# Performance work log

Measured on AMD Instinct MI355X. Metric: run time of the kernel, lower is better.

Reference implementation:

```python
import jax, jax.numpy as jnp
import numpy as np

B, Z, K, T = 4, 64, 400, 48000
CIN, COUT, KS, DIL = 128, 128, 3, 1
H = 32


def setup_inputs() -> dict:
    key = jax.random.key(0)
    ks = jax.random.split(key, 10)
    s = lambda n: 1.0 / np.sqrt(n)
    return {
        "x": jax.random.normal(ks[0], (B, CIN, T), jnp.float32),
        "z": jax.random.normal(ks[1], (B, Z, K), jnp.float32),
        # weight_model: Conv1d(Z->H, k=1), ReLU, Conv1d(H -> CIN*COUT*KS, k=1)
        "w1": jax.random.normal(ks[2], (H, Z), jnp.float32) * s(Z),
        "b1": jax.random.normal(ks[3], (H,), jnp.float32) * 0.01,
        "w2": jax.random.normal(ks[4], (CIN * COUT * KS, H), jnp.float32) * s(H),
        "b2": jax.random.normal(ks[5], (CIN * COUT * KS,), jnp.float32) * s(CIN * KS),
        # bias_model: Conv1d(Z->H, k=1), ReLU, Conv1d(H -> COUT, k=1)
        "bw1": jax.random.normal(ks[6], (H, Z), jnp.float32) * s(Z),
        "bb1": jax.random.normal(ks[7], (H,), jnp.float32) * 0.01,
        "bw2": jax.random.normal(ks[8], (COUT, H), jnp.float32) * s(H),
        "bb2": jax.random.normal(ks[9], (COUT,), jnp.float32) * 0.01,
    }


def _mlp1x1(z, wa, ba, wb, bb):
    # two pointwise Conv1d layers with ReLU in between; z: [B, Z, K]
    h = jax.nn.relu(jnp.einsum('hz,bzk->bhk', wa, z) + ba[None, :, None])
    return jnp.einsum('oh,bhk->bok', wb, h) + bb[None, :, None]


def _unfold_causal(x, ksize, dil):
    # causal im2col: tap i is x delayed by i*dil samples (left-padded with zeros)
    pad = dil * (ksize - 1)
    xp = jnp.pad(x, ((0, 0), (0, 0), (pad, 0)))
    taps = [xp[:, :, pad - i * dil: pad - i * dil + x.shape[-1]] for i in range(ksize)]
    return jnp.concatenate(taps, axis=1)  # [B, CIN*KS, T]


def reference(x, z, w1, b1, w2, b2, bw1, bb1, bw2, bb2):
    Tk = T // K  # samples per weight chunk
    xu = _unfold_causal(x, KS, DIL)                       # [B, CIN*KS, T]
    xr = xu.transpose(0, 2, 1).reshape(B * K, Tk, CIN * KS)
    w = _mlp1x1(z, w1, b1, w2, b2)                        # [B, CIN*COUT*KS, K]
    w = w.reshape(B, CIN * KS, COUT, K).transpose(0, 3, 1, 2).reshape(B * K, CIN * KS, COUT)
    bias = _mlp1x1(z, bw1, bb1, bw2, bb2)                 # [B, COUT, K]
    bias = bias.transpose(0, 2, 1).reshape(B * K, COUT)
    y = jnp.einsum('btc,bco->bto', xr, w) + bias[:, None, :]
    return y.reshape(B, T, COUT).transpose(0, 2, 1)       # [B, COUT, T]
```

## Files before the change

kernel.cpp:

```cpp
#include <hip/hip_runtime.h>
#include <stdint.h>

#define TT     48000
#define TK     120
#define NC     128
#define NA     384
#define NZ     64
#define NH     32
#define NK     400
#define NCHUNK 1600
#define MW     49152
#define XROWS  48002

typedef float f32x4 __attribute__((ext_vector_type(4)));
typedef __bf16 bf16x8 __attribute__((ext_vector_type(8)));

static __device__ __forceinline__ uint16_t f2bf(float f) {
    uint32_t x; __builtin_memcpy(&x, &f, 4);
    return (uint16_t)((x + 0x7fffu + ((x >> 16) & 1u)) >> 16);
}
static __device__ __forceinline__ uint32_t pk2(uint16_t lo, uint16_t hi) {
    return (uint32_t)lo | ((uint32_t)hi << 16);
}

__global__ __launch_bounds__(256) void k0w(
    const float* __restrict__ w2, const float* __restrict__ b2,
    uint16_t* __restrict__ w2p, float* __restrict__ b2p) {
    int m = blockIdx.x * 256 + threadIdx.x;
    int a = m >> 7, c = m & 127;
    int mp = c * NA + a;
    const float* src = w2 + (size_t)m * NH;
    uint16_t* dst = w2p + (size_t)mp * NH;
#pragma unroll
    for (int i = 0; i < NH; i += 8) {
        float4 v0 = *(const float4*)(src + i);
        float4 v1 = *(const float4*)(src + i + 4);
        uint4 o;
        o.x = pk2(f2bf(v0.x), f2bf(v0.y));
        o.y = pk2(f2bf(v0.z), f2bf(v0.w));
        o.z = pk2(f2bf(v1.x), f2bf(v1.y));
        o.w = pk2(f2bf(v1.z), f2bf(v1.w));
        *(uint4*)(dst + i) = o;
    }
    b2p[mp] = b2[m];
}

__global__ __launch_bounds__(256) void k0x(
    const float* __restrict__ x, uint16_t* __restrict__ Xt) {
    int t0 = blockIdx.x * 128, cin0 = blockIdx.y * 64, b = blockIdx.z;
    int tid = threadIdx.x;
    __shared__ __align__(16) uint16_t Lt[128][72];
    const float* xb = x + ((size_t)b * NC + cin0) * TT + t0;
    int cg = (tid & 7) * 8;
    int tq = (tid >> 3) * 4;
    uint16_t vb[4][8];
#pragma unroll
    for (int i = 0; i < 8; ++i) {
        float4 v = *(const float4*)(xb + (size_t)(cg + i) * TT + tq);
        vb[0][i] = f2bf(v.x); vb[1][i] = f2bf(v.y);
        vb[2][i] = f2bf(v.z); vb[3][i] = f2bf(v.w);
    }
#pragma unroll
    for (int j = 0; j < 4; ++j) {
        uint4 o; __builtin_memcpy(&o, vb[j], 16);
        *(uint4*)&Lt[tq + j][cg] = o;
    }
    __syncthreads();
    uint16_t* XtB = Xt + (size_t)b * XROWS * NC;
#pragma unroll
    for (int r = 0; r < 4; ++r) {
        int s = r * 256 + tid;
        int t = s >> 3, cc = s & 7;
        uint4 o = *(uint4*)&Lt[t][cc * 8];
        *(uint4*)(XtB + (size_t)(t0 + t + 2) * NC + cin0 + cc * 8) = o;
    }
    if (blockIdx.x == 0 && blockIdx.y == 0 && tid < 32)
        *(uint4*)(XtB + tid * 8) = make_uint4(0, 0, 0, 0);
}

__global__ __launch_bounds__(256) void k1_hidden(
    const float* __restrict__ z,
    const float* __restrict__ w1, const float* __restrict__ b1,
    const float* __restrict__ bw1, const float* __restrict__ bb1,
    const float* __restrict__ bw2, const float* __restrict__ bb2,
    uint16_t* __restrict__ Hb, float* __restrict__ biasws) {
    int tid = threadIdx.x, lane = tid & 63, w = tid >> 6;
    int chunk0 = blockIdx.x * 4;
    int b = chunk0 / NK;
    int k0 = chunk0 - b * NK;

    __shared__ float w1sT[64][33];
    __shared__ float bw1sT[64][33];
    __shared__ float bw2s[128][33];
    __shared__ float zs[64][4];
    __shared__ float hbs[4][33];
    __shared__ float b1s[32], bb1s[32], bb2s[128];

    {
        int row = tid >> 3, c0 = (tid & 7) * 8;
        float4 a0 = *(const float4*)(w1 + row * NZ + c0);
        float4 a1 = *(const float4*)(w1 + row * NZ + c0 + 4);
        float4 c0v = *(const float4*)(bw1 + row * NZ + c0);
        float4 c1v = *(const float4*)(bw1 + row * NZ + c0 + 4);
        const float av[8] = {a0.x,a0.y,a0.z,a0.w,a1.x,a1.y,a1.z,a1.w};
        const float cv[8] = {c0v.x,c0v.y,c0v.z,c0v.w,c1v.x,c1v.y,c1v.z,c1v.w};
#pragma unroll
        for (int j = 0; j < 8; ++j) {
            w1sT[c0 + j][row]  = av[j];
            bw1sT[c0 + j][row] = cv[j];
        }
    }
    {
        int r = tid >> 1, cb = (tid & 1) * 16;
        float4 v0 = *(const float4*)(bw2 + r * NH + cb);
        float4 v1 = *(const float4*)(bw2 + r * NH + cb + 4);
        float4 v2 = *(const float4*)(bw2 + r * NH + cb + 8);
        float4 v3 = *(const float4*)(bw2 + r * NH + cb + 12);
        const float vv[16] = {v0.x,v0.y,v0.z,v0.w,v1.x,v1.y,v1.z,v1.w,
                              v2.x,v2.y,v2.z,v2.w,v3.x,v3.y,v3.z,v3.w};
#pragma unroll
        for (int j = 0; j < 16; ++j) bw2s[r][cb + j] = vv[j];
    }
    if (tid < 64) {
        float4 zv = *(const float4*)(z + ((size_t)b * NZ + tid) * NK + k0);
        zs[tid][0] = zv.x; zs[tid][1] = zv.y; zs[tid][2] = zv.z; zs[tid][3] = zv.w;
    }
    if (tid < 32) { b1s[tid] = b1[tid]; bb1s[tid] = bb1[tid]; }
    if (tid >= 128 && tid < 256) bb2s[tid - 128] = bb2[tid - 128];
    __syncthreads();

    int chunk = chunk0 + w;
    if (lane < NH) {
        float s = b1s[lane];
#pragma unroll
        for (int i = 0; i < NZ; ++i) s = fmaf(w1sT[i][lane], zs[i][w], s);
        Hb[(size_t)chunk * NH + lane] = f2bf(fmaxf(s, 0.f));
    } else {
        int j = lane - NH;
        float s = bb1s[j];
#pragma unroll
        for (int i = 0; i < NZ; ++i) s = fmaf(bw1sT[i][j], zs[i][w], s);
        hbs[w][j] = fmaxf(s, 0.f);
    }

#pragma unroll
    for (int r = 0; r < 2; ++r) {
        int c = r * 64 + lane;
        float s = bb2s[c];
#pragma unroll
        for (int j = 0; j < NH; ++j) s = fmaf(bw2s[c][j], hbs[w][j], s);
        biasws[(size_t)chunk * NC + c] = s;
    }
}

__global__ __launch_bounds__(256) void k2_wgen(
    const uint16_t* __restrict__ w2p, const float* __restrict__ b2p,
    const uint16_t* __restrict__ Hb, uint16_t* __restrict__ Wt,
    int chunk0, int nchunk) {
    int tid = threadIdx.x, lane = tid & 63, w = tid >> 6;
    int quad = lane >> 4, li = lane & 15;
    __shared__ __align__(16) uint16_t St[4][16][68];
    int mb = blockIdx.x * 256 + w * 64;

    bf16x8 afrag[4];
    float4 bias[4];
#pragma unroll
    for (int t = 0; t < 4; ++t) {
        afrag[t] = *(const bf16x8*)(w2p + (size_t)(mb + t * 16 + li) * NH + quad * 8);
        bias[t]  = *(const float4*)(b2p + mb + t * 16 + quad * 4);
    }

    for (int g = 0; g < 10; ++g) {
        int cl0 = blockIdx.y * 160 + g * 16;
        if (cl0 >= nchunk) break;
        int cl = cl0 + li;
        if (cl >= nchunk) cl = nchunk - 1;
        bf16x8 hfrag = *(const bf16x8*)(Hb + (size_t)(chunk0 + cl) * NH + quad * 8);
#pragma unroll
        for (int t = 0; t < 4; ++t) {
            f32x4 acc = {0.f, 0.f, 0.f, 0.f};
            acc = __builtin_amdgcn_mfma_f32_16x16x32_bf16(afrag[t], hfrag, acc, 0, 0, 0);
            uint16_t p[4] = { f2bf(acc[0] + bias[t].x), f2bf(acc[1] + bias[t].y),
                              f2bf(acc[2] + bias[t].z), f2bf(acc[3] + bias[t].w) };
            uint64_t pv; __builtin_memcpy(&pv, p, 8);
            *(uint64_t*)&St[w][li][t * 16 + quad * 4] = pv;
        }
#pragma unroll
        for (int p = 0; p < 2; ++p) {
            int ch = (lane >> 3) + p * 8, part = lane & 7;
            uint4 v = *(const uint4*)&St[w][ch][part * 8];
            int cg = cl0 + ch;
            if (cg < nchunk)
                *(uint4*)(Wt + (size_t)cg * MW + mb + part * 8) = v;
        }
    }
}

__global__ __launch_bounds__(256) void k3_conv(
    const uint16_t* __restrict__ Xt, const uint16_t* __restrict__ Wt,
    const float* __restrict__ biasws, float* __restrict__ out, int chunk0) {
    int cl = blockIdx.x, chunk = chunk0 + cl;
    int b = chunk / NK, k = chunk - b * NK;
    int kbase = k * TK;
    int tid = threadIdx.x, lane = tid & 63, w = tid >> 6;
    int quad = lane >> 4, li = lane & 15;
    int tblk = (w & 1) * 64, cblk = (w >> 1) * 64;

    __shared__ __align__(16) char smem[65536];
    char* Xa  = smem;
    char* Db0 = smem + 32768;
    char* Db1 = smem + 49152;
    const uint16_t* XtB = Xt + (size_t)b * XROWS * NC;
    const uint16_t* WtC = Wt + (size_t)cl * MW;

    f32x4 acc[4][4];
#pragma unroll
    for (int i = 0; i < 4; ++i)
#pragma unroll
        for (int j = 0; j < 4; ++j) acc[i][j] = (f32x4){0.f, 0.f, 0.f, 0.f};

    auto stageD = [&](char* dst, int dks) {
#pragma unroll
        for (int j = 0; j < 4; ++j) {
            int g = (w * 4 + j) * 64 + lane;
            int c = g >> 3, sd = g & 7;
            int o = sd ^ (c & 7);
            const uint16_t* gsrc = WtC + (size_t)c * NA + dks * 64 + o * 8;
            __builtin_amdgcn_global_load_lds(
                (__attribute__((address_space(1))) void*)gsrc,
                (__attribute__((address_space(3))) void*)(dst + (w * 4 + j) * 1024),
                16, 0, 0);
        }
    };

#pragma unroll
    for (int i = 0; i < 8; ++i) {
        int brow = w * 32 + i * 4 + quad;
        const uint16_t* g = XtB + (size_t)(kbase + brow) * NC
                          + ((li ^ (brow & 15)) * 8);
        __builtin_amdgcn_global_load_lds(
            (__attribute__((address_space(1))) void*)g,
            (__attribute__((address_space(3))) void*)(Xa + (w * 32 + i * 4) * 256),
            16, 0, 0);
    }
    stageD(Db0, 0);

#pragma unroll
    for (int dk = 0; dk < 6; ++dk) {
        __syncthreads();
        if (dk < 5) stageD((dk & 1) ? Db0 : Db1, dk + 1);
        char* cur = (dk & 1) ? Db1 : Db0;
        int tap = dk >> 1;

        bf16x8 bfr[2][4];
#pragma unroll
        for (int s = 0; s < 2; ++s)
#pragma unroll
            for (int ct = 0; ct < 4; ++ct) {
                int c = cblk + ct * 16 + li;
                bfr[s][ct] = *(const bf16x8*)(cur + c * 128
                             + (((s * 4 + quad) ^ (c & 7)) << 4));
            }
#pragma unroll
        for (int s = 0; s < 2; ++s) {
            bf16x8 af[4];
#pragma unroll
            for (int tt = 0; tt < 4; ++tt) {
                int r = tblk + tt * 16 + li + 2 - tap;
                r = r > 127 ? 127 : r;
                int q = (dk & 1) * 8 + s * 4 + quad;
                af[tt] = *(const bf16x8*)(Xa + r * 256 + ((q ^ (r & 15)) << 4));
            }
#pragma unroll
            for (int tt = 0; tt < 4; ++tt)
#pragma unroll
                for (int ct = 0; ct < 4; ++ct)
                    acc[tt][ct] = __builtin_amdgcn_mfma_f32_16x16x32_bf16(
                        af[tt], bfr[s][ct], acc[tt][ct], 0, 0, 0);
        }
    }

#pragma unroll
    for (int ct = 0; ct < 4; ++ct) {
        int c = cblk + ct * 16 + li;
        float bias = biasws[(size_t)chunk * NC + c];
        float* ob = out + ((size_t)b * NC + c) * TT + kbase;
#pragma unroll
        for (int tt = 0; tt < 4; ++tt) {
            int t0v = tblk + tt * 16 + quad * 4;
            if (t0v < TK) {
                f32x4 v = acc[tt][ct];
                *(float4*)(ob + t0v) = make_float4(v[0] + bias, v[1] + bias,
                                                   v[2] + bias, v[3] + bias);
            }
        }
    }
}

extern "C" void kernel_launch(void* const* d_in, const int* in_sizes, int n_in,
                              void* d_out, int out_size, void* d_ws, size_t ws_size,
                              hipStream_t stream) {
    const float* x   = (const float*)d_in[0];
    const float* z   = (const float*)d_in[1];
    const float* w1  = (const float*)d_in[2];
    const float* b1  = (const float*)d_in[3];
    const float* w2  = (const float*)d_in[4];
    const float* b2  = (const float*)d_in[5];
    const float* bw1 = (const float*)d_in[6];
    const float* bb1 = (const float*)d_in[7];
    const float* bw2 = (const float*)d_in[8];
    const float* bb2 = (const float*)d_in[9];
    float* out = (float*)d_out;

    char* ws = (char*)d_ws;
    uint16_t* Hb     = (uint16_t*)(ws);
    float*    biasws = (float*)(ws + 102400);
    uint16_t* w2p    = (uint16_t*)(ws + 921600);
    float*    b2p    = (float*)(ws + 4067328);
    uint16_t* Xt     = (uint16_t*)(ws + 4263936);
    const size_t wt_off = 53422080;
    uint16_t* Wt     = (uint16_t*)(ws + wt_off);

    size_t avail = (ws_size > wt_off) ? (ws_size - wt_off) : 0;
    int batch = (int)(avail / ((size_t)MW * 2));
    if (batch > 800) batch = 800;
    if (batch < 1) batch = 1;

    k0w<<<MW / 256, 256, 0, stream>>>(w2, b2, w2p, b2p);
    k0x<<<dim3(TT / 128, 2, 4), 256, 0, stream>>>(x, Xt);
    k1_hidden<<<NCHUNK / 4, 256, 0, stream>>>(z, w1, b1, bw1, bb1, bw2, bb2, Hb, biasws);

    for (int c0 = 0; c0 < NCHUNK; c0 += batch) {
        int nc = NCHUNK - c0;
        if (nc > batch) nc = batch;
        dim3 g2(MW / 256, (nc + 159) / 160, 1);
        k2_wgen<<<g2, 256, 0, stream>>>(w2p, b2p, Hb, Wt, c0, nc);
        k3_conv<<<nc, 256, 0, stream>>>(Xt, Wt, biasws, out, c0);
    }
}
```

Baseline: 292.3 us.

## Fuse weight repack into wgen, triple-buffer conv weight staging, raise batch cap

Removes the separate k0w repack kernel; k2_wgen now reads fp32 w2/b2 directly with a permuted index and converts to bf16 in registers. k3_conv moves from double to triple buffering of weight tiles, using explicit vmcnt waits plus raw s_barrier so each load is issued two steps ahead. The chunk batch cap rises to the full chunk count, which can cut the number of kernel launch pairs but makes the Wt buffer larger. The extra LDS (80KB) may reduce occupancy, and the strided fp32 reads in wgen may be less efficient.

```diff
diff --git a/kernel.cpp b/kernel.cpp
--- a/kernel.cpp
+++ b/kernel.cpp
@@ -19,31 +19,6 @@
     uint32_t x; __builtin_memcpy(&x, &f, 4);
     return (uint16_t)((x + 0x7fffu + ((x >> 16) & 1u)) >> 16);
 }
-static __device__ __forceinline__ uint32_t pk2(uint16_t lo, uint16_t hi) {
-    return (uint32_t)lo | ((uint32_t)hi << 16);
-}
-
-__global__ __launch_bounds__(256) void k0w(
-    const float* __restrict__ w2, const float* __restrict__ b2,
-    uint16_t* __restrict__ w2p, float* __restrict__ b2p) {
-    int m = blockIdx.x * 256 + threadIdx.x;
-    int a = m >> 7, c = m & 127;
-    int mp = c * NA + a;
-    const float* src = w2 + (size_t)m * NH;
-    uint16_t* dst = w2p + (size_t)mp * NH;
-#pragma unroll
-    for (int i = 0; i < NH; i += 8) {
-        float4 v0 = *(const float4*)(src + i);
-        float4 v1 = *(const float4*)(src + i + 4);
-        uint4 o;
-        o.x = pk2(f2bf(v0.x), f2bf(v0.y));
-        o.y = pk2(f2bf(v0.z), f2bf(v0.w));
-        o.z = pk2(f2bf(v1.x), f2bf(v1.y));
-        o.w = pk2(f2bf(v1.z), f2bf(v1.w));
-        *(uint4*)(dst + i) = o;
-    }
-    b2p[mp] = b2[m];
-}
 
 __global__ __launch_bounds__(256) void k0x(
     const float* __restrict__ x, uint16_t* __restrict__ Xt) {
@@ -154,7 +129,7 @@
 }
 
 __global__ __launch_bounds__(256) void k2_wgen(
-    const uint16_t* __restrict__ w2p, const float* __restrict__ b2p,
+    const float* __restrict__ w2, const float* __restrict__ b2,
     const uint16_t* __restrict__ Hb, uint16_t* __restrict__ Wt,
     int chunk0, int nchunk) {
     int tid = threadIdx.x, lane = tid & 63, w = tid >> 6;
@@ -166,8 +141,21 @@
     float4 bias[4];
 #pragma unroll
     for (int t = 0; t < 4; ++t) {
-        afrag[t] = *(const bf16x8*)(w2p + (size_t)(mb + t * 16 + li) * NH + quad * 8);
-        bias[t]  = *(const float4*)(b2p + mb + t * 16 + quad * 4);
+        int mp = mb + t * 16 + li;
+        int a = mp % NA, c = mp / NA;
+        const float* src = w2 + ((size_t)a * NC + c) * NH + quad * 8;
+        float4 v0 = *(const float4*)(src);
+        float4 v1 = *(const float4*)(src + 4);
+        uint16_t tmp[8] = { f2bf(v0.x), f2bf(v0.y), f2bf(v0.z), f2bf(v0.w),
+                            f2bf(v1.x), f2bf(v1.y), f2bf(v1.z), f2bf(v1.w) };
+        __builtin_memcpy(&afrag[t], tmp, 16);
+        float bv[4];
+#pragma unroll
+        for (int r = 0; r < 4; ++r) {
+            int mpr = mb + t * 16 + quad * 4 + r;
+            bv[r] = b2[(size_t)(mpr % NA) * NC + (mpr / NA)];
+        }
+        bias[t] = make_float4(bv[0], bv[1], bv[2], bv[3]);
     }
 
     for (int g = 0; g < 10; ++g) {
@@ -206,10 +194,11 @@
     int quad = lane >> 4, li = lane & 15;
     int tblk = (w & 1) * 64, cblk = (w >> 1) * 64;
 
-    __shared__ __align__(16) char smem[65536];
+    __shared__ __align__(16) char smem[81920];
     char* Xa  = smem;
     char* Db0 = smem + 32768;
     char* Db1 = smem + 49152;
+    char* Db2 = smem + 65536;
     const uint16_t* XtB = Xt + (size_t)b * XROWS * NC;
     const uint16_t* WtC = Wt + (size_t)cl * MW;
 
@@ -244,12 +233,20 @@
             16, 0, 0);
     }
     stageD(Db0, 0);
+    stageD(Db1, 1);
 
 #pragma unroll
     for (int dk = 0; dk < 6; ++dk) {
-        __syncthreads();
-        if (dk < 5) stageD((dk & 1) ? Db0 : Db1, dk + 1);
-        char* cur = (dk & 1) ? Db1 : Db0;
+        if (dk < 5) asm volatile("s_waitcnt vmcnt(4)" ::: "memory");
+        else        asm volatile("s_waitcnt vmcnt(0)" ::: "memory");
+        __builtin_amdgcn_s_barrier();
+        __builtin_amdgcn_sched_barrier(0);
+        if (dk < 4) {
+            int sel = (dk + 2) % 3;
+            stageD(sel == 0 ? Db0 : (sel == 1 ? Db1 : Db2), dk + 2);
+        }
+        int cs = dk % 3;
+        char* cur = cs == 0 ? Db0 : (cs == 1 ? Db1 : Db2);
         int tap = dk >> 1;
 
         bf16x8 bfr[2][4];
@@ -315,18 +312,15 @@
     char* ws = (char*)d_ws;
     uint16_t* Hb     = (uint16_t*)(ws);
     float*    biasws = (float*)(ws + 102400);
-    uint16_t* w2p    = (uint16_t*)(ws + 921600);
-    float*    b2p    = (float*)(ws + 4067328);
-    uint16_t* Xt     = (uint16_t*)(ws + 4263936);
-    const size_t wt_off = 53422080;
+    uint16_t* Xt     = (uint16_t*)(ws + 921600);
+    const size_t wt_off = 50079744;
     uint16_t* Wt     = (uint16_t*)(ws + wt_off);
 
     size_t avail = (ws_size > wt_off) ? (ws_size - wt_off) : 0;
     int batch = (int)(avail / ((size_t)MW * 2));
-    if (batch > 800) batch = 800;
+    if (batch > NCHUNK) batch = NCHUNK;
     if (batch < 1) batch = 1;
 
-    k0w<<<MW / 256, 256, 0, stream>>>(w2, b2, w2p, b2p);
     k0x<<<dim3(TT / 128, 2, 4), 256, 0, stream>>>(x, Xt);
     k1_hidden<<<NCHUNK / 4, 256, 0, stream>>>(z, w1, b1, bw1, bb1, bw2, bb2, Hb, biasws);
 
@@ -334,7 +328,7 @@
         int nc = NCHUNK - c0;
         if (nc > batch) nc = batch;
         dim3 g2(MW / 256, (nc + 159) / 160, 1);
-        k2_wgen<<<g2, 256, 0, stream>>>(w2p, b2p, Hb, Wt, c0, nc);
+        k2_wgen<<<g2, 256, 0, stream>>>(w2, b2, Hb, Wt, c0, nc);
         k3_conv<<<nc, 256, 0, stream>>>(Xt, Wt, biasws, out, c0);
     }
 }
```

Measured after the change: 299.5 us. 1.02x slower.
